# Kernel optimization log

Measured on AMD Instinct MI355X. Metric: run time of the kernel, lower is better.

The kernel has to match this reference:

```python
import jax, jax.numpy as jnp
import numpy as np
from jax import lax

RATIOS = np.array([0.5, 1.0, 2.0], dtype=np.float32)
SCALES = np.array([8.0, 16.0, 32.0], dtype=np.float32)
BASE = 16.0
FEAT_STRIDE = 16
N_PRE_NMS = 6000
N_POST_NMS = 300
NMS_THRESH = 0.7
MIN_SIZE = 16.0
SCALE = 1.0
NEG_INF = -1e30


def generate_anchor_base():
    # (y1, x1, y2, x2) anchors centered at (BASE/2, BASE/2)
    h = BASE * SCALES[None, :] * np.sqrt(RATIOS)[:, None]          # [3,3]
    w = BASE * SCALES[None, :] * np.sqrt(1.0 / RATIOS)[:, None]
    cy = cx = BASE / 2.0
    ab = np.stack([cy - h / 2, cx - w / 2, cy + h / 2, cx + w / 2], axis=-1)
    return jnp.asarray(ab.reshape(-1, 4), dtype=jnp.float32)       # [9,4]


def enumerate_shift_anchor(anchor_base, hh, ww):
    sy = jnp.arange(hh, dtype=jnp.float32) * FEAT_STRIDE
    sx = jnp.arange(ww, dtype=jnp.float32) * FEAT_STRIDE
    mx, my = jnp.meshgrid(sx, sy)                                   # np.meshgrid(shift_x, shift_y)
    shift = jnp.stack([my.ravel(), mx.ravel(), my.ravel(), mx.ravel()], axis=1)  # [K,4]
    return (shift[:, None, :] + anchor_base[None, :, :]).reshape(-1, 4)          # [K*9,4]


def conv2d(x, w, b, pad):
    y = lax.conv_general_dilated(x, w, (1, 1), [(pad, pad), (pad, pad)],
                                 dimension_numbers=('NCHW', 'OIHW', 'NCHW'))
    return y + b[None, :, None, None]


def loc2bbox(anchor, loc):
    h = anchor[:, 2] - anchor[:, 0]
    w = anchor[:, 3] - anchor[:, 1]
    cy = anchor[:, 0] + 0.5 * h
    cx = anchor[:, 1] + 0.5 * w
    dy, dx, dh, dw = loc[:, 0], loc[:, 1], loc[:, 2], loc[:, 3]
    ncy = dy * h + cy
    ncx = dx * w + cx
    nh = jnp.exp(dh) * h
    nw = jnp.exp(dw) * w
    return jnp.stack([ncy - 0.5 * nh, ncx - 0.5 * nw, ncy + 0.5 * nh, ncx + 0.5 * nw], axis=1)


def nms_fixed(boxes, scores):
    # boxes [P,4] already score-sorted desc; greedy NMS, fixed N_POST_NMS outputs (zero-padded)
    def body(i, state):
        sc, keep = state
        idx = jnp.argmax(sc)
        valid = sc[idx] > NEG_INF / 2
        keep = keep.at[i].set(jnp.where(valid, idx, -1))
        box = boxes[idx]
        tl = jnp.maximum(box[:2], boxes[:, :2])
        br = jnp.minimum(box[2:], boxes[:, 2:])
        wh = jnp.clip(br - tl, 0.0)
        inter = wh[:, 0] * wh[:, 1]
        a1 = (box[2] - box[0]) * (box[3] - box[1])
        a2 = (boxes[:, 2] - boxes[:, 0]) * (boxes[:, 3] - boxes[:, 1])
        iou = inter / jnp.maximum(a1 + a2 - inter, 1e-6)
        sc = jnp.where(iou > NMS_THRESH, NEG_INF, sc)
        sc = sc.at[idx].set(NEG_INF)
        return sc, keep
    keep = jnp.full((N_POST_NMS,), -1, dtype=jnp.int32)
    _, keep = lax.fori_loop(0, N_POST_NMS, body, (scores, keep))
    rois = boxes[jnp.maximum(keep, 0)]
    return jnp.where(keep[:, None] >= 0, rois, 0.0)                # [N_POST,4]


def propose_one(loc, fg_score, anchor, img_h, img_w):
    roi = loc2bbox(anchor, loc)                                     # [A,4]
    roi = jnp.stack([jnp.clip(roi[:, 0], 0.0, img_h),
                     jnp.clip(roi[:, 1], 0.0, img_w),
                     jnp.clip(roi[:, 2], 0.0, img_h),
                     jnp.clip(roi[:, 3], 0.0, img_w)], axis=1)
    min_size = MIN_SIZE * SCALE
    hs = roi[:, 2] - roi[:, 0]
    ws = roi[:, 3] - roi[:, 1]
    valid = (hs >= min_size) & (ws >= min_size)
    sc = jnp.where(valid, fg_score, NEG_INF)
    top_sc, top_idx = lax.top_k(sc, N_PRE_NMS)
    return nms_fixed(roi[top_idx], top_sc)


def reference(x, conv1_w, conv1_b, score_w, score_b, loc_w, loc_b, img_h, img_w):
    n, _, hh, ww = x.shape
    anchor = enumerate_shift_anchor(generate_anchor_base(), hh, ww)  # [hh*ww*9,4]
    n_anchor = anchor.shape[0] // (hh * ww)
    feat = jax.nn.relu(conv2d(x, conv1_w, conv1_b, 1))
    rpn_locs = conv2d(feat, loc_w, loc_b, 0).transpose(0, 2, 3, 1).reshape(n, -1, 4)
    rpn_scores = conv2d(feat, score_w, score_b, 0).transpose(0, 2, 3, 1)
    soft = jax.nn.softmax(rpn_scores.reshape(n, hh, ww, n_anchor, 2), axis=4)
    rpn_fg = soft[..., 1].reshape(n, -1)
    rpn_scores = rpn_scores.reshape(n, -1, 2)
    rois = jax.vmap(lambda l, s: propose_one(l, s, anchor, float(img_h), float(img_w)))(rpn_locs, rpn_fg)
    return rpn_locs, rpn_scores, rois, anchor


def setup_inputs() -> dict:
    key = jax.random.key(0)
    ks = jax.random.split(key, 4)
    return {
        'x': jax.random.normal(ks[0], (4, 512, 64, 64), dtype=jnp.float32),
        'conv1_w': jax.random.normal(ks[1], (512, 512, 3, 3), dtype=jnp.float32) * 0.01,
        'conv1_b': jnp.zeros((512,), dtype=jnp.float32),
        'score_w': jax.random.normal(ks[2], (18, 512, 1, 1), dtype=jnp.float32) * 0.01,
        'score_b': jnp.zeros((18,), dtype=jnp.float32),
        'loc_w': jax.random.normal(ks[3], (36, 512, 1, 1), dtype=jnp.float32) * 0.01,
        'loc_b': jnp.zeros((36,), dtype=jnp.float32),
        'img_h': 1024,
        'img_w': 1024,
    }
```

## Files before the change

### kernel.cpp

```cpp
#include <hip/hip_runtime.h>
#include <stdint.h>

typedef unsigned int u32;
typedef unsigned long long u64;
typedef unsigned short ushort_t;

#define NANCH 36864
#define NPRE 6000
#define NPOST 300
#define CAP 6144
#define NKEEP 6000
#define MROWS 6016
#define MW 192
#define NEG_INF_F (-1e30f)

typedef __attribute__((ext_vector_type(8))) __bf16 bf8_t;
typedef __attribute__((ext_vector_type(8))) unsigned short us8_t;
typedef __attribute__((ext_vector_type(16))) float f32x16;

union pun8 { us8_t u; bf8_t b; };

__device__ __forceinline__ u32 fsort(float f) {
    u32 u = __float_as_uint(f);
    return (u & 0x80000000u) ? ~u : (u | 0x80000000u);
}

__device__ __forceinline__ unsigned short f2bf(float f) {
    u32 u = __float_as_uint(f);
    u32 r = (u + 0x7FFFu + ((u >> 16) & 1u)) >> 16;
    return (unsigned short)r;
}
__device__ __forceinline__ float bf2f(unsigned short s) {
    return __uint_as_float(((u32)s) << 16);
}

__device__ __forceinline__ int ctz32(u32 x) {
    return __builtin_ctz(x ? x : 1u);
}

__device__ __forceinline__ void gl_lds16(const void* g, void* l) {
    __builtin_amdgcn_global_load_lds(
        (const __attribute__((address_space(1))) unsigned int*)(g),
        (__attribute__((address_space(3))) unsigned int*)(l), 16, 0, 0);
}

#define XS_SPL ((size_t)4 * 32 * 64 * 2 * 64)

__global__ void setup_k(const float* __restrict__ w1, const float* __restrict__ sw,
                        const float* __restrict__ lw, const float* __restrict__ x,
                        ushort_t* __restrict__ Wp, ushort_t* __restrict__ Xs,
                        float* __restrict__ wt1, float* __restrict__ out_anchor,
                        u32* __restrict__ cnt) {
    __shared__ float xt[16][2][64];
    const int bid = blockIdx.x;
    const int tid = threadIdx.x;
    if (bid < 128) {
        int T = bid * 256 + tid;
        int lane31 = T & 31;
        int cot    = (T >> 5) & 15;
        int khalf  = (T >> 9) & 1;
        int kc     = T >> 10;
        int co  = cot * 32 + lane31;
        int ci0 = kc * 16 + khalf * 8;
        int lane = lane31 + khalf * 32;
        const float* wr = w1 + (size_t)co * 4608 + (size_t)ci0 * 9;
        us8_t* P = (us8_t*)Wp;
        const size_t sa_stride = (size_t)9 * 32 * 16 * 64;
#pragma unroll
        for (int t = 0; t < 9; ++t) {
            us8_t vh, vm, vl;
#pragma unroll
            for (int j = 0; j < 8; ++j) {
                float v = wr[j * 9 + t];
                unsigned short h = f2bf(v); float r1 = v - bf2f(h);
                unsigned short m = f2bf(r1); float r2 = r1 - bf2f(m);
                vh[j] = h; vm[j] = m; vl[j] = f2bf(r2);
            }
            size_t base = ((((size_t)t) * 32 + kc) * 16 + cot) * 64 + lane;
            P[base] = vh;
            P[base + sa_stride] = vm;
            P[base + 2 * sa_stride] = vl;
        }
    } else if (bid < 256) {
        int i = (bid - 128) * 256 + tid;
        int ci = i >> 6;
        int ch = i & 63;
        float v = 0.f;
        if (ch < 18) v = sw[ch * 512 + ci];
        else if (ch < 54) v = lw[(ch - 18) * 512 + ci];
        wt1[i] = v;
    } else if (bid < 400) {
        int i = (bid - 256) * 256 + tid;
        if (i < NANCH) {
            int p = i / 9, a = i - p * 9;
            int y = p / 64, xq = p - y * 64;
            int r = a / 3, s = a - r * 3;
            const float rat[3] = {0.5f, 1.f, 2.f};
            const float scl[3] = {8.f, 16.f, 32.f};
            float hh = 16.f * scl[s] * sqrtf(rat[r]);
            float wwv = 16.f * scl[s] * sqrtf(1.f / rat[r]);
            float ab0 = 8.f - 0.5f * hh, ab1 = 8.f - 0.5f * wwv;
            float ab2 = 8.f + 0.5f * hh, ab3 = 8.f + 0.5f * wwv;
            float sy = 16.f * (float)y, sx = 16.f * (float)xq;
            ((float4*)out_anchor)[i] = make_float4(sy + ab0, sx + ab1, sy + ab2, sx + ab3);
        }
    } else if (bid == 400) {
        if (tid < 8) cnt[tid] = 0u;
    } else {
        int pk = bid - 401;
        int img = pk >> 5, kc = pk & 31;
        us8_t* XP = (us8_t*)Xs;
        for (int h2 = 0; h2 < 32; ++h2) {
#pragma unroll
            for (int i = 0; i < 8; ++i) {
                int idx = i * 256 + tid;
                int ci = idx >> 7, rem = idx & 127, hrow = rem >> 6, w = rem & 63;
                int h = h2 * 2 + hrow;
                xt[ci][hrow][w] = x[(((size_t)img * 512 + kc * 16 + ci) * 64 + h) * 64 + w];
            }
            __syncthreads();
            {
                int hrow = tid >> 7, st = tid & 127, half = st >> 6, w = st & 63;
                int h = h2 * 2 + hrow;
                us8_t vh, vm, vl;
#pragma unroll
                for (int j = 0; j < 8; ++j) {
                    float v = xt[half * 8 + j][hrow][w];
                    unsigned short hb = f2bf(v); float r1 = v - bf2f(hb);
                    unsigned short mb = f2bf(r1); float r2 = r1 - bf2f(mb);
                    vh[j] = hb; vm[j] = mb; vl[j] = f2bf(r2);
                }
                size_t ob = ((((size_t)img * 32 + kc) * 64 + h) * 2 + half) * 64 + w;
                XP[ob] = vh;
                XP[XS_SPL + ob] = vm;
                XP[2 * XS_SPL + ob] = vl;
            }
            __syncthreads();
        }
    }
}

__global__ __launch_bounds__(256, 2) void conv_mfma_k(const ushort_t* __restrict__ Xs,
                                                      const ushort_t* __restrict__ Wp,
                                                      const float* __restrict__ bias,
                                                      float* __restrict__ feat) {
    __shared__ __align__(16) unsigned short xs[12672];

    const int bid = blockIdx.x;
    const int xcd = bid & 7;
    const int rest = bid >> 3;
    const int coq = xcd >> 1;
    const int g = (xcd & 1) * 64 + rest;
    const int fimg = g >> 5;
    const int hp = g & 31;
    const int h0 = hp * 2;

    const int tid = threadIdx.x;
    const int lane = tid & 63;
    const int wv = tid >> 6;
    const int r = wv & 1;
    const int coh = (wv >> 1);
    const int col31 = lane & 31;
    const int halfk = lane >> 5;

    {
        u32* p = (u32*)xs;
        for (int i = tid; i < 6336; i += 256) p[i] = 0u;
    }
    __syncthreads();

    f32x16 acc[4];
#pragma unroll
    for (int q = 0; q < 4; ++q)
#pragma unroll
        for (int i = 0; i < 16; ++i) acc[q][i] = 0.f;

    const us8_t* Pw = (const us8_t*)Wp;
    const size_t sa_stride = (size_t)9 * 32 * 16 * 64;
    static const int sal[6] = {0, 0, 1, 0, 1, 2};
    static const int sbl[6] = {0, 1, 0, 2, 1, 0};

    for (int kc = 0; kc < 32; ++kc) {
#pragma unroll
        for (int q = 0; q < 6; ++q) {
            int i = wv * 6 + q;
            int split = i >> 3;
            int rem = i & 7;
            int rr = rem >> 1;
            int half = rem & 1;
            int gh = h0 + rr - 1;
            if ((unsigned)gh < 64u) {
                const char* src = (const char*)Xs +
                    (((((size_t)split * 4 + fimg) * 32 + kc) * 64 + gh) * 2 + half) * 1024 +
                    (size_t)lane * 16;
                void* dst = (void*)&xs[(((split * 2 + half) * 4 + rr) * 66 + 1) * 8];
                gl_lds16(src, dst);
            }
        }
        __syncthreads();

#pragma unroll
        for (int t = 0; t < 9; ++t) {
            const int kh = t / 3, kw = t - kh * 3;
            pun8 Bf[3][2];
#pragma unroll
            for (int sb = 0; sb < 3; ++sb)
#pragma unroll
                for (int ps = 0; ps < 2; ++ps)
                    Bf[sb][ps].u = *(const us8_t*)&xs[(((sb * 2 + halfk) * 4 + (r + kh)) * 66 +
                                                      (ps * 32 + col31 + kw)) * 8];
            pun8 Af[3][2];
            size_t abase = (((size_t)t * 32 + kc) * 16 + coq * 4 + coh * 2) * 64 + lane;
#pragma unroll
            for (int sa = 0; sa < 3; ++sa)
#pragma unroll
                for (int cs = 0; cs < 2; ++cs)
                    Af[sa][cs].u = Pw[sa * sa_stride + abase + (size_t)cs * 64];
#pragma unroll
            for (int pp = 0; pp < 6; ++pp) {
                const int sa = sal[pp], sb = sbl[pp];
#pragma unroll
                for (int cs = 0; cs < 2; ++cs)
#pragma unroll
                    for (int ps = 0; ps < 2; ++ps)
                        acc[cs * 2 + ps] = __builtin_amdgcn_mfma_f32_32x32x16_bf16(
                            Af[sa][cs].b, Bf[sb][ps].b, acc[cs * 2 + ps], 0, 0, 0);
            }
        }
        __syncthreads();
    }

#pragma unroll
    for (int cs = 0; cs < 2; ++cs)
#pragma unroll
        for (int ps = 0; ps < 2; ++ps)
#pragma unroll
            for (int i = 0; i < 16; ++i) {
                int m = (i & 3) + 8 * (i >> 2) + 4 * halfk;
                int co = coq * 128 + coh * 64 + cs * 32 + m;
                float v = acc[cs * 2 + ps][i] + bias[co];
                v = v > 0.f ? v : 0.f;
                feat[(((size_t)fimg * 512 + co) * 64 + (h0 + r)) * 64 + (ps * 32 + col31)] = v;
            }
}

__global__ __launch_bounds__(256, 2) void conv_fb_k(const float* __restrict__ x,
                                                    const ushort_t* __restrict__ Wp,
                                                    const float* __restrict__ bias,
                                                    float* __restrict__ feat,
                                                    int img_base) {
    __shared__ __align__(16) unsigned short xsb[3 * 6336];

    const int bid = blockIdx.x;
    const int xcd = bid & 7;
    const int rest = bid >> 3;
    const int rest_max = gridDim.x >> 3;
    const int coq = xcd >> 1;
    const int g = (xcd & 1) * rest_max + rest;
    const int fimg = g >> 5;
    const int hp = g & 31;
    const int n = img_base + fimg;
    const int h0 = hp * 2;

    const int tid = threadIdx.x;
    const int lane = tid & 63;
    const int wv = tid >> 6;
    const int r = wv & 1;
    const int coh = (wv >> 1);
    const int col31 = lane & 31;
    const int halfk = lane >> 5;

    f32x16 acc[4];
#pragma unroll
    for (int q = 0; q < 4; ++q)
#pragma unroll
        for (int i = 0; i < 16; ++i) acc[q][i] = 0.f;

    const us8_t* Pw = (const us8_t*)Wp;
    const size_t sa_stride = (size_t)9 * 32 * 16 * 64;
    static const int sal[6] = {0, 0, 1, 0, 1, 2};
    static const int sbl[6] = {0, 1, 0, 2, 1, 0};

    for (int kc = 0; kc < 32; ++kc) {
        for (int e = tid; e < 528; e += 256) {
            int half = e & 1;
            int rc = e >> 1;
            int rr = rc / 66;
            int cc = rc - rr * 66;
            int gr = h0 + rr - 1;
            int gc = cc - 1;
            bool inb = ((unsigned)gr < 64u) && ((unsigned)gc < 64u);
            int ci0 = kc * 16 + half * 8;
            const float* xp = x + ((((size_t)n * 512 + ci0) * 64 + gr) * 64 + gc);
            us8_t vh, vm, vl;
#pragma unroll
            for (int j = 0; j < 8; ++j) {
                float v = inb ? xp[(size_t)j * 4096] : 0.f;
                unsigned short h = f2bf(v); float r1 = v - bf2f(h);
                unsigned short m = f2bf(r1); float r2 = r1 - bf2f(m);
                vh[j] = h; vm[j] = m; vl[j] = f2bf(r2);
            }
            int off = (rr * 66 + cc) * 24 + half * 8;
            *(us8_t*)&xsb[off] = vh;
            *(us8_t*)&xsb[6336 + off] = vm;
            *(us8_t*)&xsb[12672 + off] = vl;
        }
        __syncthreads();

#pragma unroll
        for (int t = 0; t < 9; ++t) {
            const int kh = t / 3, kw = t - kh * 3;
            pun8 Bf[3][2];
            int boff0 = ((r + kh) * 66 + (col31 + kw)) * 24 + halfk * 8;
#pragma unroll
            for (int sb = 0; sb < 3; ++sb)
#pragma unroll
                for (int ps = 0; ps < 2; ++ps)
                    Bf[sb][ps].u = *(const us8_t*)&xsb[sb * 6336 + boff0 + ps * (32 * 24)];
            pun8 Af[3][2];
            size_t abase = (((size_t)t * 32 + kc) * 16 + coq * 4 + coh * 2) * 64 + lane;
#pragma unroll
            for (int sa = 0; sa < 3; ++sa)
#pragma unroll
                for (int cs = 0; cs < 2; ++cs)
                    Af[sa][cs].u = Pw[sa * sa_stride + abase + (size_t)cs * 64];
#pragma unroll
            for (int pp = 0; pp < 6; ++pp) {
                const int sa = sal[pp], sb = sbl[pp];
#pragma unroll
                for (int cs = 0; cs < 2; ++cs)
#pragma unroll
                    for (int ps = 0; ps < 2; ++ps)
                        acc[cs * 2 + ps] = __builtin_amdgcn_mfma_f32_32x32x16_bf16(
                            Af[sa][cs].b, Bf[sb][ps].b, acc[cs * 2 + ps], 0, 0, 0);
            }
        }
        __syncthreads();
    }

#pragma unroll
    for (int cs = 0; cs < 2; ++cs)
#pragma unroll
        for (int ps = 0; ps < 2; ++ps)
#pragma unroll
            for (int i = 0; i < 16; ++i) {
                int m = (i & 3) + 8 * (i >> 2) + 4 * halfk;
                int co = coq * 128 + coh * 64 + cs * 32 + m;
                float v = acc[cs * 2 + ps][i] + bias[co];
                v = v > 0.f ? v : 0.f;
                feat[(((size_t)fimg * 512 + co) * 64 + (h0 + r)) * 64 + (ps * 32 + col31)] = v;
            }
}

__global__ __launch_bounds__(64) void head_k(const float* __restrict__ feat,
                                             const float* __restrict__ wt1,
                                             const float* __restrict__ sb,
                                             const float* __restrict__ lb,
                                             const int* __restrict__ img_h,
                                             const int* __restrict__ img_w,
                                             float* __restrict__ out_loc,
                                             float* __restrict__ out_sc,
                                             float* __restrict__ boxes,
                                             float* __restrict__ scf,
                                             int img_base) {
    const int lane = threadIdx.x;
    const int row = blockIdx.x;
    const int fimg = blockIdx.y;
    const int n = img_base + fimg;

    float acc[56];
#pragma unroll
    for (int i = 0; i < 56; i++) acc[i] = 0.f;

    for (int ci = 0; ci < 512; ++ci) {
        float f = feat[(((size_t)fimg * 512 + ci) * 64 + row) * 64 + lane];
        const float4* wp = (const float4*)(wt1 + ci * 64);
#pragma unroll
        for (int q = 0; q < 14; q++) {
            float4 w4 = wp[q];
            acc[q * 4 + 0] = fmaf(f, w4.x, acc[q * 4 + 0]);
            acc[q * 4 + 1] = fmaf(f, w4.y, acc[q * 4 + 1]);
            acc[q * 4 + 2] = fmaf(f, w4.z, acc[q * 4 + 2]);
            acc[q * 4 + 3] = fmaf(f, w4.w, acc[q * 4 + 3]);
        }
    }

    float ihf = (float)img_h[0];
    float iwf = (float)img_w[0];
    int p = row * 64 + lane;
    size_t base = (size_t)n * NANCH + (size_t)p * 9;
    float sy = 16.f * (float)row;
    float sx = 16.f * (float)lane;
    const float rat[3] = {0.5f, 1.f, 2.f};
    const float scl[3] = {8.f, 16.f, 32.f};

#pragma unroll
    for (int a = 0; a < 9; a++) {
        int rr = a / 3, s = a % 3;
        float hh = 16.f * scl[s] * sqrtf(rat[rr]);
        float wwv = 16.f * scl[s] * sqrtf(1.f / rat[rr]);
        float ab0 = 8.f - 0.5f * hh, ab1 = 8.f - 0.5f * wwv;
        float ab2 = 8.f + 0.5f * hh, ab3 = 8.f + 0.5f * wwv;
        float a0 = sy + ab0, a1c = sx + ab1, a2 = sy + ab2, a3 = sx + ab3;

        float s0 = acc[a * 2 + 0] + sb[a * 2 + 0];
        float s1 = acc[a * 2 + 1] + sb[a * 2 + 1];
        ((float2*)out_sc)[base + a] = make_float2(s0, s1);
        float m = fmaxf(s0, s1);
        float e0 = expf(s0 - m), e1 = expf(s1 - m);
        float fg = e1 / (e0 + e1);

        float dy = acc[18 + a * 4 + 0] + lb[a * 4 + 0];
        float dx = acc[18 + a * 4 + 1] + lb[a * 4 + 1];
        float dh = acc[18 + a * 4 + 2] + lb[a * 4 + 2];
        float dw = acc[18 + a * 4 + 3] + lb[a * 4 + 3];
        ((float4*)out_loc)[base + a] = make_float4(dy, dx, dh, dw);

        float h_ = a2 - a0, w_ = a3 - a1c;
        float cy = a0 + 0.5f * h_, cx = a1c + 0.5f * w_;
        float ncy = dy * h_ + cy, ncx = dx * w_ + cx;
        float nh = expf(dh) * h_, nw = expf(dw) * w_;
        float y1 = ncy - 0.5f * nh, x1 = ncx - 0.5f * nw;
        float y2 = ncy + 0.5f * nh, x2 = ncx + 0.5f * nw;
        y1 = fminf(fmaxf(y1, 0.f), ihf);
        x1 = fminf(fmaxf(x1, 0.f), iwf);
        y2 = fminf(fmaxf(y2, 0.f), ihf);
        x2 = fminf(fmaxf(x2, 0.f), iwf);
        float hs = y2 - y1, wsz = x2 - x1;
        bool valid = (hs >= 16.f) && (wsz >= 16.f);
        ((float4*)boxes)[base + a] = make_float4(y1, x1, y2, x2);
        scf[base + a] = valid ? fg : NEG_INF_F;
    }
}

__global__ __launch_bounds__(1024) void radix_k(const float* __restrict__ scf, u32* __restrict__ uT) {
    const int b = blockIdx.x;
    const int tid = threadIdx.x;
    const float* s = scf + (size_t)b * NANCH;
    __shared__ u32 hist[256];
    __shared__ u32 sel_prefix;
    __shared__ int sel_rank;
    if (tid == 0) { sel_prefix = 0u; sel_rank = NPRE; }
    __syncthreads();
    for (int p = 3; p >= 0; --p) {
        for (int i = tid; i < 256; i += 1024) hist[i] = 0u;
        __syncthreads();
        u32 prefix = sel_prefix;
        u32 highmask = (p == 3) ? 0u : (0xFFFFFFFFu << ((p + 1) * 8));
        for (int i = tid; i < NANCH; i += 1024) {
            u32 u = fsort(s[i]);
            if ((u & highmask) == prefix)
                atomicAdd(&hist[(u >> (p * 8)) & 255], 1u);
        }
        __syncthreads();
        if (tid == 0) {
            int r = sel_rank;
            u32 accum = 0;
            int bsel = 0;
            for (int bb = 255; bb >= 0; --bb) {
                accum += hist[bb];
                if ((int)accum >= r) {
                    bsel = bb;
                    sel_rank = r - (int)(accum - hist[bb]);
                    break;
                }
            }
            sel_prefix = prefix | ((u32)bsel << (p * 8));
        }
        __syncthreads();
    }
    if (tid == 0) uT[b] = sel_prefix;
}

__global__ void compact_k(const float* __restrict__ scf, const u32* __restrict__ uT,
                          u32* __restrict__ cnt, u32* __restrict__ cidx) {
    int b = blockIdx.y;
    int i = blockIdx.x * 256 + threadIdx.x;
    float s = scf[(size_t)b * NANCH + i];
    u32 u = fsort(s);
    if (u >= uT[b] && s > -5e29f) {
        u32 p = atomicAdd(&cnt[b], 1u);
        if (p < CAP) cidx[(size_t)b * CAP + p] = (u32)i;
    }
}

__global__ __launch_bounds__(1024) void sort_k(const float* __restrict__ scf,
                                               const float* __restrict__ boxes,
                                               u32* __restrict__ cnt,
                                               const u32* __restrict__ cidx,
                                               float4* __restrict__ sbox) {
    __shared__ u64 sk[8192];
    const int b = blockIdx.x;
    const int tid = threadIdx.x;
    int count = (int)cnt[b];
    if (count > CAP) count = CAP;

    for (int i = tid; i < 8192; i += 1024) {
        u64 key = 0ull;
        if (i < count) {
            u32 idx = cidx[(size_t)b * CAP + i];
            u32 u = fsort(scf[(size_t)b * NANCH + idx]);
            key = ((u64)u << 32) | (u64)(0xFFFFFFFFu - idx);
        }
        sk[i] = key;
    }

    for (int k = 2; k <= 8192; k <<= 1) {
        for (int j = k >> 1; j > 0; j >>= 1) {
            __syncthreads();
            for (int i = tid; i < 8192; i += 1024) {
                int p = i ^ j;
                if (p > i) {
                    bool up = (i & k) == 0;
                    u64 a = sk[i], c = sk[p];
                    bool sw = up ? (a < c) : (a > c);
                    if (sw) { sk[i] = c; sk[p] = a; }
                }
            }
        }
    }
    __syncthreads();

    int S = count < NKEEP ? count : NKEEP;
    if (tid == 0) cnt[4 + b] = (u32)S;
    const float4* Bx = (const float4*)boxes;
    for (int i = tid; i < S; i += 1024) {
        u32 idx = 0xFFFFFFFFu - (u32)(sk[i] & 0xFFFFFFFFull);
        sbox[(size_t)b * CAP + i] = Bx[(size_t)b * NANCH + idx];
    }
}

__global__ __launch_bounds__(256) void mask_k(const float4* __restrict__ sbox,
                                              const u32* __restrict__ cnt,
                                              u32* __restrict__ mask) {
    __shared__ float4 rb[64];
    __shared__ float ra[64];
    const int tile = blockIdx.x;
    const int b = blockIdx.y;
    const int tid = threadIdx.x;
    const int lane = tid & 63;
    const int wv = tid >> 6;
    const int r0 = tile * 64;

    if (tid < 64) {
        float4 v = sbox[(size_t)b * CAP + (r0 + tid)];
        rb[tid] = v;
        ra[tid] = (v.z - v.x) * (v.w - v.y);
    }
    __syncthreads();

    for (int chunk = (tile >> 2); chunk < 24; ++chunk) {
        int c = chunk * 256 + tid;
        float4 cb = sbox[(size_t)b * CAP + c];
        float a2 = (cb.z - cb.x) * (cb.w - cb.y);
        u64 mine = 0ull;
#pragma unroll 4
        for (int r = 0; r < 64; ++r) {
            float4 rr = rb[r];
            float ty = fmaxf(rr.x, cb.x);
            float tx = fmaxf(rr.y, cb.y);
            float by = fminf(rr.z, cb.z);
            float bx = fminf(rr.w, cb.w);
            float ih = fmaxf(by - ty, 0.f);
            float iw = fmaxf(bx - tx, 0.f);
            float inter = ih * iw;
            float iou = inter / fmaxf(ra[r] + a2 - inter, 1e-6f);
            u64 bal = __ballot(iou > 0.7f);
            if (lane == r) mine = bal;
        }
        int row = r0 + lane;
        u64* dst = (u64*)(mask + ((size_t)b * MROWS + row) * MW);
        dst[chunk * 4 + wv] = mine;
    }
}

__global__ __launch_bounds__(1024) void scan_k(const u32* __restrict__ mask,
                                               const float4* __restrict__ sbox,
                                               const u32* __restrict__ cnt,
                                               u32* __restrict__ sink,
                                               float4* __restrict__ out_rois) {
    const int b = blockIdx.x;
    const int tid = threadIdx.x;
    const int wv = tid >> 6;
    const int lane = tid & 63;
    const int S = (int)cnt[4 + b];

    __shared__ int keep[NPOST];
    __shared__ int posS;
    volatile int* vpos = &posS;
    if (tid == 0) *vpos = 0;
    __syncthreads();

    const u32* mbase = mask + (size_t)b * MROWS * MW;

    if (wv == 0) {
        u32 a0, a1, a2v;
        {
            int w;
            w = lane;       a0  = (w * 32 + 32 <= S) ? 0xFFFFFFFFu : ((w * 32 < S) ? ((1u << (S - w * 32)) - 1u) : 0u);
            w = 64 + lane;  a1  = (w * 32 + 32 <= S) ? 0xFFFFFFFFu : ((w * 32 < S) ? ((1u << (S - w * 32)) - 1u) : 0u);
            w = 128 + lane; a2v = (w * 32 + 32 <= S) ? 0xFFFFFFFFu : ((w * 32 < S) ? ((1u << (S - w * 32)) - 1u) : 0u);
        }

        int it = 0;
        while (it < NPOST) {
            int j;
            u64 b0 = __ballot(a0 != 0u);
            if (b0) {
                int L = __builtin_ctzll(b0);
                int cv = (lane << 5) + ctz32(a0);
                j = __shfl(cv, L);
            } else {
                u64 b1 = __ballot(a1 != 0u);
                if (b1) {
                    int L = __builtin_ctzll(b1);
                    int cv = ((64 + lane) << 5) + ctz32(a1);
                    j = __shfl(cv, L);
                } else {
                    u64 b2 = __ballot(a2v != 0u);
                    if (!b2) break;
                    int L = __builtin_ctzll(b2);
                    int cv = ((128 + lane) << 5) + ctz32(a2v);
                    j = __shfl(cv, L);
                }
            }
            if (lane == 0) { keep[it] = j; *vpos = j; }
            ++it;

            int wj = j >> 5;
            u32 bit = 1u << (j & 31);
            if (wj == lane) a0 &= ~bit;
            else if (wj == 64 + lane) a1 &= ~bit;
            else if (wj == 128 + lane) a2v &= ~bit;

            const u32* row = mbase + (size_t)j * MW;
            u32 m0 = row[lane];
            u32 m1 = row[64 + lane];
            u32 m2 = row[128 + lane];
            a0 &= ~m0; a1 &= ~m1; a2v &= ~m2;
        }

        if (lane == 0) *vpos = (1 << 28);

        int total = it;
        for (int i = lane; i < NPOST; i += 64) {
            float4 v = make_float4(0.f, 0.f, 0.f, 0.f);
            if (i < total) v = sbox[(size_t)b * CAP + keep[i]];
            out_rois[(size_t)b * NPOST + i] = v;
        }
    } else {
        u32 dummy = 0u;
        const int W = 2048;
        for (int r = wv - 1; r < MROWS; r += 15) {
            int sp = 0;
            while (*vpos + W <= r && sp < 65536) { __builtin_amdgcn_s_sleep(2); ++sp; }
            if (*vpos >= (1 << 27)) break;
            const u32* row = mbase + (size_t)r * MW;
            dummy += row[lane] + row[64 + lane] + row[128 + lane];
        }
        if (dummy == 0xDEADBEEFu) sink[b] = dummy;
    }
}

extern "C" void kernel_launch(void* const* d_in, const int* in_sizes, int n_in,
                              void* d_out, int out_size, void* d_ws, size_t ws_size,
                              hipStream_t stream) {
    const float* x  = (const float*)d_in[0];
    const float* w1 = (const float*)d_in[1];
    const float* b1 = (const float*)d_in[2];
    const float* sw = (const float*)d_in[3];
    const float* sb = (const float*)d_in[4];
    const float* lw = (const float*)d_in[5];
    const float* lb = (const float*)d_in[6];
    const int* ih   = (const int*)d_in[7];
    const int* iw   = (const int*)d_in[8];
    float* out = (float*)d_out;

    char* ws = (char*)d_ws;
    const size_t NEED_XL  = 101614080;
    const size_t NEED_BIG = 51413504;
    const int mode = (ws_size >= NEED_XL) ? 2 : (ws_size >= NEED_BIG ? 1 : 0);

    ushort_t* Wp  = (ushort_t*)(ws);
    ushort_t* Xs  = (ushort_t*)(ws + 14155776);
    float* feat   = (float*)(ws + (mode == 2 ? 64487424 : 14286848));
    u32* mask     = (u32*)(ws);
    const size_t RB = (mode == 2) ? 98041856 : (mode == 1 ? 47841280 : 31064064);
    float* wt1    = (float*)(ws + RB);
    float* boxes  = (float*)(ws + RB + 131072);
    float* scf    = (float*)(ws + RB + 2490368);
    u32* uT       = (u32*)(ws + RB + 3080192);
    u32* cnt      = (u32*)(ws + RB + 3080448);
    u32* cidx     = (u32*)(ws + RB + 3080704);
    float4* sbox  = (float4*)(ws + RB + 3179008);

    float* out_loc = out;
    float* out_sc  = out + 589824;
    float4* out_roi = (float4*)(out + 884736);
    float* out_anc = out + 889536;

    hipLaunchKernelGGL(setup_k, dim3(mode == 2 ? 529 : 401), dim3(256), 0, stream,
                       w1, sw, lw, x, Wp, Xs, wt1, out_anc, cnt);

    if (mode == 2) {
        hipLaunchKernelGGL(conv_mfma_k, dim3(512), dim3(256), 0, stream, (const ushort_t*)Xs, Wp, b1, feat);
        hipLaunchKernelGGL(head_k, dim3(64, 4), dim3(64), 0, stream, feat, wt1, sb, lb, ih, iw,
                           out_loc, out_sc, boxes, scf, 0);
    } else if (mode == 1) {
        hipLaunchKernelGGL(conv_fb_k, dim3(512), dim3(256), 0, stream, x, Wp, b1, feat, 0);
        hipLaunchKernelGGL(head_k, dim3(64, 4), dim3(64), 0, stream, feat, wt1, sb, lb, ih, iw,
                           out_loc, out_sc, boxes, scf, 0);
    } else {
        for (int pass = 0; pass < 2; ++pass) {
            hipLaunchKernelGGL(conv_fb_k, dim3(256), dim3(256), 0, stream, x, Wp, b1, feat, pass * 2);
            hipLaunchKernelGGL(head_k, dim3(64, 2), dim3(64), 0, stream, feat, wt1, sb, lb, ih, iw,
                               out_loc, out_sc, boxes, scf, pass * 2);
        }
    }

    hipLaunchKernelGGL(radix_k, dim3(4), dim3(1024), 0, stream, scf, uT);
    hipLaunchKernelGGL(compact_k, dim3(144, 4), dim3(256), 0, stream, scf, uT, cnt, cidx);
    hipLaunchKernelGGL(sort_k, dim3(4), dim3(1024), 0, stream, scf, boxes, cnt, cidx, sbox);
    hipLaunchKernelGGL(mask_k, dim3(94, 4), dim3(256), 0, stream, sbox, cnt, mask);
    hipLaunchKernelGGL(scan_k, dim3(4), dim3(1024), 0, stream, mask, sbox, cnt, cidx, out_roi);
}
```

Baseline: 1.118 ms.

## Fuse radix select, compaction and sort; split head channel reduction across four waves

Merges the radix threshold select, global-atomic compaction and bitonic sort into one per-image kernel. The compaction now goes straight into shared memory through a shared-memory atomic counter, which removes two launches and the global cidx round trip. The radix histogram is privatized per wave to cut shared atomic contention. The head kernel now uses 256 threads, with each wave summing a quarter of the input channels before a shared-memory reduction, so it keeps more waves in flight. The cost is a larger shared footprint, and the ordering of the float additions in the head changes.

Result: faster. 1.022 ms (-8.6%).

```diff
diff --git a/kernel.cpp b/kernel.cpp
--- a/kernel.cpp
+++ b/kernel.cpp
@@ -24,7 +24,6 @@
     u32 u = __float_as_uint(f);
     return (u & 0x80000000u) ? ~u : (u | 0x80000000u);
 }
-
 __device__ __forceinline__ unsigned short f2bf(float f) {
     u32 u = __float_as_uint(f);
     u32 r = (u + 0x7FFFu + ((u >> 16) & 1u)) >> 16;
@@ -33,11 +32,9 @@
 __device__ __forceinline__ float bf2f(unsigned short s) {
     return __uint_as_float(((u32)s) << 16);
 }
-
 __device__ __forceinline__ int ctz32(u32 x) {
     return __builtin_ctz(x ? x : 1u);
 }
-
 __device__ __forceinline__ void gl_lds16(const void* g, void* l) {
     __builtin_amdgcn_global_load_lds(
         (const __attribute__((address_space(1))) unsigned int*)(g),
@@ -45,12 +42,12 @@
 }
 
 #define XS_SPL ((size_t)4 * 32 * 64 * 2 * 64)
+#define WP_SPL ((size_t)9 * 32 * 16 * 64)
 
 __global__ void setup_k(const float* __restrict__ w1, const float* __restrict__ sw,
                         const float* __restrict__ lw, const float* __restrict__ x,
                         ushort_t* __restrict__ Wp, ushort_t* __restrict__ Xs,
-                        float* __restrict__ wt1, float* __restrict__ out_anchor,
-                        u32* __restrict__ cnt) {
+                        float* __restrict__ wt1, float* __restrict__ out_anchor) {
     __shared__ float xt[16][2][64];
     const int bid = blockIdx.x;
     const int tid = threadIdx.x;
@@ -65,7 +62,6 @@
         int lane = lane31 + khalf * 32;
         const float* wr = w1 + (size_t)co * 4608 + (size_t)ci0 * 9;
         us8_t* P = (us8_t*)Wp;
-        const size_t sa_stride = (size_t)9 * 32 * 16 * 64;
 #pragma unroll
         for (int t = 0; t < 9; ++t) {
             us8_t vh, vm, vl;
@@ -78,8 +74,8 @@
             }
             size_t base = ((((size_t)t) * 32 + kc) * 16 + cot) * 64 + lane;
             P[base] = vh;
-            P[base + sa_stride] = vm;
-            P[base + 2 * sa_stride] = vl;
+            P[base + WP_SPL] = vm;
+            P[base + 2 * WP_SPL] = vl;
         }
     } else if (bid < 256) {
         int i = (bid - 128) * 256 + tid;
@@ -104,10 +100,8 @@
             float sy = 16.f * (float)y, sx = 16.f * (float)xq;
             ((float4*)out_anchor)[i] = make_float4(sy + ab0, sx + ab1, sy + ab2, sx + ab3);
         }
-    } else if (bid == 400) {
-        if (tid < 8) cnt[tid] = 0u;
     } else {
-        int pk = bid - 401;
+        int pk = bid - 400;
         int img = pk >> 5, kc = pk & 31;
         us8_t* XP = (us8_t*)Xs;
         for (int h2 = 0; h2 < 32; ++h2) {
@@ -176,7 +170,6 @@
         for (int i = 0; i < 16; ++i) acc[q][i] = 0.f;
 
     const us8_t* Pw = (const us8_t*)Wp;
-    const size_t sa_stride = (size_t)9 * 32 * 16 * 64;
     static const int sal[6] = {0, 0, 1, 0, 1, 2};
     static const int sbl[6] = {0, 1, 0, 2, 1, 0};
 
@@ -215,7 +208,7 @@
             for (int sa = 0; sa < 3; ++sa)
 #pragma unroll
                 for (int cs = 0; cs < 2; ++cs)
-                    Af[sa][cs].u = Pw[sa * sa_stride + abase + (size_t)cs * 64];
+                    Af[sa][cs].u = Pw[sa * WP_SPL + abase + (size_t)cs * 64];
 #pragma unroll
             for (int pp = 0; pp < 6; ++pp) {
                 const int sa = sal[pp], sb = sbl[pp];
@@ -277,7 +270,6 @@
         for (int i = 0; i < 16; ++i) acc[q][i] = 0.f;
 
     const us8_t* Pw = (const us8_t*)Wp;
-    const size_t sa_stride = (size_t)9 * 32 * 16 * 64;
     static const int sal[6] = {0, 0, 1, 0, 1, 2};
     static const int sbl[6] = {0, 1, 0, 2, 1, 0};
 
@@ -323,7 +315,7 @@
             for (int sa = 0; sa < 3; ++sa)
 #pragma unroll
                 for (int cs = 0; cs < 2; ++cs)
-                    Af[sa][cs].u = Pw[sa * sa_stride + abase + (size_t)cs * 64];
+                    Af[sa][cs].u = Pw[sa * WP_SPL + abase + (size_t)cs * 64];
 #pragma unroll
             for (int pp = 0; pp < 6; ++pp) {
                 const int sa = sal[pp], sb = sbl[pp];
@@ -352,18 +344,21 @@
             }
 }
 
-__global__ __launch_bounds__(64) void head_k(const float* __restrict__ feat,
-                                             const float* __restrict__ wt1,
-                                             const float* __restrict__ sb,
-                                             const float* __restrict__ lb,
-                                             const int* __restrict__ img_h,
-                                             const int* __restrict__ img_w,
-                                             float* __restrict__ out_loc,
-                                             float* __restrict__ out_sc,
-                                             float* __restrict__ boxes,
-                                             float* __restrict__ scf,
-                                             int img_base) {
-    const int lane = threadIdx.x;
+__global__ __launch_bounds__(256) void head_k(const float* __restrict__ feat,
+                                              const float* __restrict__ wt1,
+                                              const float* __restrict__ sb,
+                                              const float* __restrict__ lb,
+                                              const int* __restrict__ img_h,
+                                              const int* __restrict__ img_w,
+                                              float* __restrict__ out_loc,
+                                              float* __restrict__ out_sc,
+                                              float* __restrict__ boxes,
+                                              float* __restrict__ scf,
+                                              int img_base) {
+    __shared__ float red[3][56][64];
+    const int tid = threadIdx.x;
+    const int lane = tid & 63;
+    const int wv = tid >> 6;
     const int row = blockIdx.x;
     const int fimg = blockIdx.y;
     const int n = img_base + fimg;
@@ -372,7 +367,7 @@
 #pragma unroll
     for (int i = 0; i < 56; i++) acc[i] = 0.f;
 
-    for (int ci = 0; ci < 512; ++ci) {
+    for (int ci = wv * 128; ci < wv * 128 + 128; ++ci) {
         float f = feat[(((size_t)fimg * 512 + ci) * 64 + row) * 64 + lane];
         const float4* wp = (const float4*)(wt1 + ci * 64);
 #pragma unroll
@@ -384,6 +379,17 @@
             acc[q * 4 + 3] = fmaf(f, w4.w, acc[q * 4 + 3]);
         }
     }
+
+    if (wv > 0) {
+#pragma unroll
+        for (int i = 0; i < 56; i++) red[wv - 1][i][lane] = acc[i];
+    }
+    __syncthreads();
+    if (wv != 0) return;
+
+#pragma unroll
+    for (int i = 0; i < 56; i++)
+        acc[i] = ((acc[i] + red[0][i][lane]) + red[1][i][lane]) + red[2][i][lane];
 
     float ihf = (float)img_h[0];
     float iwf = (float)img_w[0];
@@ -433,77 +439,75 @@
     }
 }
 
-__global__ __launch_bounds__(1024) void radix_k(const float* __restrict__ scf, u32* __restrict__ uT) {
+__global__ __launch_bounds__(1024) void rss_k(const float* __restrict__ scf,
+                                              const float* __restrict__ boxes,
+                                              u32* __restrict__ cnt,
+                                              float4* __restrict__ sbox) {
+    __shared__ u64 sk[8192];
+    __shared__ u32 histT[256];
+    __shared__ u32 prefixS;
+    __shared__ int rankS;
+    __shared__ int cntS;
+
     const int b = blockIdx.x;
     const int tid = threadIdx.x;
+    const int wv = tid >> 6;
     const float* s = scf + (size_t)b * NANCH;
-    __shared__ u32 hist[256];
-    __shared__ u32 sel_prefix;
-    __shared__ int sel_rank;
-    if (tid == 0) { sel_prefix = 0u; sel_rank = NPRE; }
+    u32* hist = (u32*)sk;
+
+    if (tid == 0) { prefixS = 0u; rankS = NPRE; }
     __syncthreads();
+
     for (int p = 3; p >= 0; --p) {
-        for (int i = tid; i < 256; i += 1024) hist[i] = 0u;
+        for (int i = tid; i < 4096; i += 1024) hist[i] = 0u;
         __syncthreads();
-        u32 prefix = sel_prefix;
+        u32 prefix = prefixS;
         u32 highmask = (p == 3) ? 0u : (0xFFFFFFFFu << ((p + 1) * 8));
         for (int i = tid; i < NANCH; i += 1024) {
             u32 u = fsort(s[i]);
             if ((u & highmask) == prefix)
-                atomicAdd(&hist[(u >> (p * 8)) & 255], 1u);
+                atomicAdd(&hist[wv * 256 + ((u >> (p * 8)) & 255)], 1u);
+        }
+        __syncthreads();
+        if (tid < 256) {
+            u32 t = 0;
+#pragma unroll
+            for (int w = 0; w < 16; ++w) t += hist[w * 256 + tid];
+            histT[tid] = t;
         }
         __syncthreads();
         if (tid == 0) {
-            int r = sel_rank;
+            int r = rankS;
             u32 accum = 0;
             int bsel = 0;
             for (int bb = 255; bb >= 0; --bb) {
-                accum += hist[bb];
+                accum += histT[bb];
                 if ((int)accum >= r) {
                     bsel = bb;
-                    sel_rank = r - (int)(accum - hist[bb]);
+                    rankS = r - (int)(accum - histT[bb]);
                     break;
                 }
             }
-            sel_prefix = prefix | ((u32)bsel << (p * 8));
+            prefixS = prefixS | ((u32)bsel << (p * 8));
+            cntS = 0;
         }
         __syncthreads();
     }
-    if (tid == 0) uT[b] = sel_prefix;
-}
-
-__global__ void compact_k(const float* __restrict__ scf, const u32* __restrict__ uT,
-                          u32* __restrict__ cnt, u32* __restrict__ cidx) {
-    int b = blockIdx.y;
-    int i = blockIdx.x * 256 + threadIdx.x;
-    float s = scf[(size_t)b * NANCH + i];
-    u32 u = fsort(s);
-    if (u >= uT[b] && s > -5e29f) {
-        u32 p = atomicAdd(&cnt[b], 1u);
-        if (p < CAP) cidx[(size_t)b * CAP + p] = (u32)i;
-    }
-}
-
-__global__ __launch_bounds__(1024) void sort_k(const float* __restrict__ scf,
-                                               const float* __restrict__ boxes,
-                                               u32* __restrict__ cnt,
-                                               const u32* __restrict__ cidx,
-                                               float4* __restrict__ sbox) {
-    __shared__ u64 sk[8192];
-    const int b = blockIdx.x;
-    const int tid = threadIdx.x;
-    int count = (int)cnt[b];
-    if (count > CAP) count = CAP;
-
-    for (int i = tid; i < 8192; i += 1024) {
-        u64 key = 0ull;
-        if (i < count) {
-            u32 idx = cidx[(size_t)b * CAP + i];
-            u32 u = fsort(scf[(size_t)b * NANCH + idx]);
-            key = ((u64)u << 32) | (u64)(0xFFFFFFFFu - idx);
-        }
-        sk[i] = key;
-    }
+
+    u32 uTv = prefixS;
+    for (int i = tid; i < NANCH; i += 1024) {
+        float sv = s[i];
+        u32 u = fsort(sv);
+        if (u >= uTv && sv > -5e29f) {
+            int pos = atomicAdd(&cntS, 1);
+            if (pos < 8192)
+                sk[pos] = ((u64)u << 32) | (u64)(0xFFFFFFFFu - (u32)i);
+        }
+    }
+    __syncthreads();
+    int count = cntS;
+    if (count > 8192) count = 8192;
+    for (int i = count + tid; i < 8192; i += 1024) sk[i] = 0ull;
 
     for (int k = 2; k <= 8192; k <<= 1) {
         for (int j = k >> 1; j > 0; j >>= 1) {
@@ -531,7 +535,6 @@
 }
 
 __global__ __launch_bounds__(256) void mask_k(const float4* __restrict__ sbox,
-                                              const u32* __restrict__ cnt,
                                               u32* __restrict__ mask) {
     __shared__ float4 rb[64];
     __shared__ float ra[64];
@@ -677,8 +680,8 @@
     float* out = (float*)d_out;
 
     char* ws = (char*)d_ws;
-    const size_t NEED_XL  = 101614080;
-    const size_t NEED_BIG = 51413504;
+    const size_t NEED_XL  = 101515776;
+    const size_t NEED_BIG = 51315200;
     const int mode = (ws_size >= NEED_XL) ? 2 : (ws_size >= NEED_BIG ? 1 : 0);
 
     ushort_t* Wp  = (ushort_t*)(ws);
@@ -689,38 +692,35 @@
     float* wt1    = (float*)(ws + RB);
     float* boxes  = (float*)(ws + RB + 131072);
     float* scf    = (float*)(ws + RB + 2490368);
-    u32* uT       = (u32*)(ws + RB + 3080192);
-    u32* cnt      = (u32*)(ws + RB + 3080448);
-    u32* cidx     = (u32*)(ws + RB + 3080704);
-    float4* sbox  = (float4*)(ws + RB + 3179008);
+    u32* cnt      = (u32*)(ws + RB + 3080192);
+    u32* sink     = (u32*)(ws + RB + 3080448);
+    float4* sbox  = (float4*)(ws + RB + 3080704);
 
     float* out_loc = out;
     float* out_sc  = out + 589824;
     float4* out_roi = (float4*)(out + 884736);
     float* out_anc = out + 889536;
 
-    hipLaunchKernelGGL(setup_k, dim3(mode == 2 ? 529 : 401), dim3(256), 0, stream,
-                       w1, sw, lw, x, Wp, Xs, wt1, out_anc, cnt);
+    hipLaunchKernelGGL(setup_k, dim3(mode == 2 ? 528 : 400), dim3(256), 0, stream,
+                       w1, sw, lw, x, Wp, Xs, wt1, out_anc);
 
     if (mode == 2) {
         hipLaunchKernelGGL(conv_mfma_k, dim3(512), dim3(256), 0, stream, (const ushort_t*)Xs, Wp, b1, feat);
-        hipLaunchKernelGGL(head_k, dim3(64, 4), dim3(64), 0, stream, feat, wt1, sb, lb, ih, iw,
+        hipLaunchKernelGGL(head_k, dim3(64, 4), dim3(256), 0, stream, feat, wt1, sb, lb, ih, iw,
                            out_loc, out_sc, boxes, scf, 0);
     } else if (mode == 1) {
         hipLaunchKernelGGL(conv_fb_k, dim3(512), dim3(256), 0, stream, x, Wp, b1, feat, 0);
-        hipLaunchKernelGGL(head_k, dim3(64, 4), dim3(64), 0, stream, feat, wt1, sb, lb, ih, iw,
+        hipLaunchKernelGGL(head_k, dim3(64, 4), dim3(256), 0, stream, feat, wt1, sb, lb, ih, iw,
                            out_loc, out_sc, boxes, scf, 0);
     } else {
         for (int pass = 0; pass < 2; ++pass) {
             hipLaunchKernelGGL(conv_fb_k, dim3(256), dim3(256), 0, stream, x, Wp, b1, feat, pass * 2);
-            hipLaunchKernelGGL(head_k, dim3(64, 2), dim3(64), 0, stream, feat, wt1, sb, lb, ih, iw,
+            hipLaunchKernelGGL(head_k, dim3(64, 2), dim3(256), 0, stream, feat, wt1, sb, lb, ih, iw,
                                out_loc, out_sc, boxes, scf, pass * 2);
         }
     }
 
-    hipLaunchKernelGGL(radix_k, dim3(4), dim3(1024), 0, stream, scf, uT);
-    hipLaunchKernelGGL(compact_k, dim3(144, 4), dim3(256), 0, stream, scf, uT, cnt, cidx);
-    hipLaunchKernelGGL(sort_k, dim3(4), dim3(1024), 0, stream, scf, boxes, cnt, cidx, sbox);
-    hipLaunchKernelGGL(mask_k, dim3(94, 4), dim3(256), 0, stream, sbox, cnt, mask);
-    hipLaunchKernelGGL(scan_k, dim3(4), dim3(1024), 0, stream, mask, sbox, cnt, cidx, out_roi);
-}
+    hipLaunchKernelGGL(rss_k, dim3(4), dim3(1024), 0, stream, scf, boxes, cnt, sbox);
+    hipLaunchKernelGGL(mask_k, dim3(94, 4), dim3(256), 0, stream, sbox, mask);
+    hipLaunchKernelGGL(scan_k, dim3(4), dim3(1024), 0, stream, mask, sbox, cnt, sink, out_roi);
+}
```
